# Kernel tuning notes

Measured on AMD Instinct MI355X. Metric: run time of the kernel, lower is better.

## Reference

```python
import jax, jax.numpy as jnp
import numpy as np

B, T, D, H = 4, 2048, 1024, 16
HD = D // H

def setup_inputs() -> dict:
    key = jax.random.key(0)
    ks = jax.random.split(key, 12)
    s = 0.02
    return {
        "query": jax.random.normal(ks[0], (B, T, D), dtype=jnp.float32),
        "key_": jax.random.normal(ks[1], (B, T, D), dtype=jnp.float32),
        "value": jax.random.normal(ks[2], (B, T, D), dtype=jnp.float32),
        "attention_mask": jnp.zeros((B, T, T), dtype=bool),
        "Wq": jax.random.normal(ks[3], (D, D), dtype=jnp.float32) * s,
        "bq": jnp.zeros((D,), dtype=jnp.float32),
        "Wk": jax.random.normal(ks[4], (D, D), dtype=jnp.float32) * s,
        "bk": jnp.zeros((D,), dtype=jnp.float32),
        "Wv": jax.random.normal(ks[5], (D, D), dtype=jnp.float32) * s,
        "bv": jnp.zeros((D,), dtype=jnp.float32),
        "Wo": jax.random.normal(ks[6], (D, D), dtype=jnp.float32) * s,
        "bo": jnp.zeros((D,), dtype=jnp.float32),
    }

def reference(query, key_, value, attention_mask, Wq, bq, Wk, bk, Wv, bv, Wo, bo):
    scale = 1.0 / jnp.sqrt(jnp.float32(HD))
    # projections (torch Linear: x @ W.T + b), split heads -> [B, H, T, HD]
    q = (query @ Wq.T + bq).reshape(B, T, H, HD).transpose(0, 2, 1, 3)
    k = (key_ @ Wk.T + bk).reshape(B, T, H, HD).transpose(0, 2, 1, 3)
    v = (value @ Wv.T + bv).reshape(B, T, H, HD).transpose(0, 2, 1, 3)
    scores = jnp.einsum('bhqd,bhkd->bhqk', q, k) * scale  # [B,H,T,T]
    mask = attention_mask[:, None, :, :]  # [B,1,T,T], True = masked
    scores = jnp.where(mask, -jnp.inf, scores)
    attn = jax.nn.softmax(scores, axis=-1)
    out = jnp.einsum('bhqk,bhkd->bhqd', attn, v)  # [B,H,T,HD]
    out = out.transpose(0, 2, 1, 3).reshape(B, T, D)
    return out @ Wo.T + bo
```

## Files before the change

### kernel.cpp

```cpp
#include <hip/hip_runtime.h>
#include <hip/hip_bf16.h>
#include <math.h>


typedef short bf16x8 __attribute__((ext_vector_type(8)));
typedef short bf16x4 __attribute__((ext_vector_type(4)));
typedef float f32x4  __attribute__((ext_vector_type(4)));
typedef float f32x16 __attribute__((ext_vector_type(16)));
typedef unsigned u32x4v __attribute__((ext_vector_type(4)));

#define DEV __device__ __forceinline__

DEV short f2bf(float f) {
    union { float f; unsigned u; } x; x.f = f;
    unsigned r = x.u + 0x7fffu + ((x.u >> 16) & 1u);
    return (short)(r >> 16);
}

DEV unsigned cvtpk(float lo, float hi) {
    unsigned r;
    asm("v_cvt_pk_bf16_f32 %0, %1, %2" : "=v"(r) : "v"(lo), "v"(hi));
    return r;
}

DEV void pl32swap(unsigned &a, unsigned &b) {
    asm volatile("v_permlane32_swap_b32 %0, %1" : "+v"(a), "+v"(b));
}

DEV float fexp2(float x) {
    float r;
    asm("v_exp_f32 %0, %1\n\ts_nop 0" : "=v"(r) : "v"(x));
    return r;
}

DEV void gload16(const void* g, void* lds_wave_base) {
    __builtin_amdgcn_global_load_lds(
        (const __attribute__((address_space(1))) void*)g,
        (__attribute__((address_space(3))) void*)lds_wave_base, 16, 0, 0);
}

DEV f32x4 mfma16(bf16x8 a, bf16x8 b, f32x4 c) {
    return __builtin_amdgcn_mfma_f32_16x16x32_bf16(a, b, c, 0, 0, 0);
}
DEV f32x16 mfma32(bf16x8 a, bf16x8 b, f32x16 c) {
    return __builtin_amdgcn_mfma_f32_32x32x16_bf16(a, b, c, 0, 0, 0);
}

__global__ __launch_bounds__(256) void cvt_one(const float* __restrict__ in,
                                               short* __restrict__ out) {
    int i = (blockIdx.x * 256 + threadIdx.x) * 8;
    f32x4 a = *(const f32x4*)(in + i);
    f32x4 b = *(const f32x4*)(in + i + 4);
    union { unsigned u[4]; bf16x8 v; } p;
    p.u[0] = cvtpk(a[0], a[1]); p.u[1] = cvtpk(a[2], a[3]);
    p.u[2] = cvtpk(b[0], b[1]); p.u[3] = cvtpk(b[2], b[3]);
    *(bf16x8*)(out + i) = p.v;
}

__global__ __launch_bounds__(256) void cvt_w4(
    const float* __restrict__ a, const float* __restrict__ b,
    const float* __restrict__ c, const float* __restrict__ d,
    short* __restrict__ oa, short* __restrict__ ob,
    short* __restrict__ oc, short* __restrict__ od) {
    const int sel = blockIdx.x >> 9;
    const float* in = sel == 0 ? a : sel == 1 ? b : sel == 2 ? c : d;
    short* out      = sel == 0 ? oa : sel == 1 ? ob : sel == 2 ? oc : od;
    int i = ((blockIdx.x & 511) * 256 + threadIdx.x) * 8;
    f32x4 x = *(const f32x4*)(in + i);
    f32x4 y = *(const f32x4*)(in + i + 4);
    union { unsigned u[4]; bf16x8 v; } p;
    p.u[0] = cvtpk(x[0], x[1]); p.u[1] = cvtpk(x[2], x[3]);
    p.u[2] = cvtpk(y[0], y[1]); p.u[3] = cvtpk(y[2], y[3]);
    *(bf16x8*)(out + i) = p.v;
}

template<int EPI>
__global__ __launch_bounds__(256) void gemm_bt(
    const short* __restrict__ A, const short* __restrict__ W,
    const float* __restrict__ bias, void* __restrict__ Cp, float epiScale)
{
    __shared__ short Alds[2][4096];
    __shared__ short Blds[2][4096];

    const int t = threadIdx.x;
    const int wave = t >> 6, lane = t & 63;
    const int lr = lane & 15, lg = lane >> 4;
    const int wg = (blockIdx.x & 7) * 64 + (blockIdx.x >> 3);
    const int m0 = (wg >> 3) * 128, n0 = (wg & 7) * 128;
    const int wr = wave >> 1, wc = wave & 1;

    const int o0 = t * 16,        kb0 = o0 >> 11, row0 = (o0 >> 4) & 127;
    const int o1 = 4096 + t * 16, kb1 = o1 >> 11, row1 = (o1 >> 4) & 127;
    const short* As0 = A + (size_t)(m0 + row0) * 1024 + kb0 * 8;
    const short* As1 = A + (size_t)(m0 + row1) * 1024 + kb1 * 8;
    const short* Ws0 = W + (size_t)(n0 + row0) * 1024 + kb0 * 8;
    const short* Ws1 = W + (size_t)(n0 + row1) * 1024 + kb1 * 8;

    auto stage = [&](short* dA, short* dB, int k0) {
        gload16(As0 + k0, (char*)dA + wave * 1024);
        gload16(As1 + k0, (char*)dA + 4096 + wave * 1024);
        gload16(Ws0 + k0, (char*)dB + wave * 1024);
        gload16(Ws1 + k0, (char*)dB + 4096 + wave * 1024);
    };

    f32x4 acc[4][4] = {};

    stage(Alds[0], Blds[0], 0);

    auto kstep = [&](int ts, int BUF) {
        if (ts < 31) {
            stage(Alds[BUF ^ 1], Blds[BUF ^ 1], (ts + 1) * 32);
            asm volatile("s_waitcnt vmcnt(4)" ::: "memory");
        } else {
            asm volatile("s_waitcnt vmcnt(0)" ::: "memory");
        }
        __builtin_amdgcn_s_barrier();
        bf16x8 af[4], bfr[4];
        #pragma unroll
        for (int mi = 0; mi < 4; mi++)
            af[mi] = *(const bf16x8*)(Alds[BUF] + lg * 1024 + (wr * 64 + mi * 16 + lr) * 8);
        #pragma unroll
        for (int ni = 0; ni < 4; ni++)
            bfr[ni] = *(const bf16x8*)(Blds[BUF] + lg * 1024 + (wc * 64 + ni * 16 + lr) * 8);
        #pragma unroll
        for (int mi = 0; mi < 4; mi++)
            #pragma unroll
            for (int ni = 0; ni < 4; ni++)
                acc[mi][ni] = mfma16(af[mi], bfr[ni], acc[mi][ni]);
        __builtin_amdgcn_s_barrier();
    };

    #pragma unroll 1
    for (int it = 0; it < 16; ++it) { kstep(2 * it, 0); kstep(2 * it + 1, 1); }

    #pragma unroll
    for (int mi = 0; mi < 4; mi++) {
        #pragma unroll
        for (int ni = 0; ni < 4; ni++) {
            const int n      = n0 + wc * 64 + ni * 16 + lr;
            const int m_base = m0 + wr * 64 + mi * 16 + lg * 4;
            const float bv   = bias[n];
            f32x4 a = acc[mi][ni];
            if constexpr (EPI == 0) {
                short* C = (short*)Cp;
                #pragma unroll
                for (int r = 0; r < 4; r++)
                    C[(size_t)(m_base + r) * 1024 + n] = f2bf((a[r] + bv) * epiScale);
            } else if constexpr (EPI == 2) {
                short* C = (short*)Cp;
                const int b = m_base >> 11, tt = m_base & 2047;
                bf16x4 p;
                #pragma unroll
                for (int r = 0; r < 4; r++) p[r] = f2bf(a[r] + bv);
                *(bf16x4*)(C + (size_t)b * 2097152 + (size_t)n * 2048 + tt) = p;
            } else {
                float* C = (float*)Cp;
                #pragma unroll
                for (int r = 0; r < 4; r++)
                    C[(size_t)(m_base + r) * 1024 + n] = a[r] + bv;
            }
        }
    }
}

__global__ __launch_bounds__(256) void mask_scan(const unsigned char* __restrict__ mask,
                                                 unsigned char* __restrict__ flags) {
    __shared__ int anyk[32];
    const int t = threadIdx.x, kt = t & 31, g = t >> 5;
    const int b = blockIdx.x >> 6, qt = blockIdx.x & 63;
    if (t < 32) anyk[t] = 0;
    __syncthreads();
    unsigned acc = 0;
    const unsigned char* base = mask + ((size_t)b * 2048 + qt * 32 + g * 4) * 2048 + kt * 64;
    #pragma unroll
    for (int rr = 0; rr < 4; rr++) {
        const uint4* p = (const uint4*)(base + (size_t)rr * 2048);
        #pragma unroll
        for (int s = 0; s < 4; s++) { uint4 v = p[s]; acc |= v.x | v.y | v.z | v.w; }
    }
    if (acc) anyk[kt] = 1;
    __syncthreads();
    if (t < 32) flags[((size_t)b * 64 + qt) * 32 + t] = (unsigned char)anyk[t];
}

__global__ __launch_bounds__(256, 2) void attn_fwd3(
    const short* __restrict__ Q, const short* __restrict__ K,
    const short* __restrict__ Vt, const unsigned char* __restrict__ mask,
    const unsigned char* __restrict__ flags, short* __restrict__ O)
{
    __shared__ short lds[2][2][8192];

    const int t = threadIdx.x, wave = t >> 6, lane = t & 63;
    const int j31 = lane & 31, hi = lane >> 5;

    const int raw = blockIdx.x;
    const int wg  = (raw & 7) * 128 + (raw >> 3);
    const int qblk = wg & 15, bh = wg >> 4;
    const int h = bh & 15, b = bh >> 4;
    const int q0 = qblk * 128 + wave * 32;

    bf16x8 qf[4];
    {
        const short* qp = Q + ((size_t)b * 2048 + q0 + j31) * 1024 + h * 64 + hi * 8;
        #pragma unroll
        for (int ck = 0; ck < 4; ck++) qf[ck] = *(const bf16x8*)(qp + ck * 16);
    }
    unsigned long long fmask;
    {
        unsigned char fb = flags[((size_t)b * 64 + qblk * 4 + wave) * 32 + j31];
        fmask = __ballot(fb != 0);
    }
    bf16x8 onesv;
    #pragma unroll
    for (int i = 0; i < 8; i++) onesv[i] = (short)0x3F80;

    const short* Kg = K + ((size_t)b * 2048) * 1024 + h * 64;
    const short* Vg = Vt + (size_t)b * 2097152 + (size_t)h * 64 * 2048;

    auto stage = [&](short* dK, short* dV, int tk) {
        #pragma unroll
        for (int i = 0; i < 4; i++) {
            const int s = i * 256 + t;
            const int rK = s >> 3, cK = ((s & 7) ^ (rK & 7)) * 8;
            gload16(Kg + (size_t)(tk + rK) * 1024 + cK, dK + i * 2048 + wave * 512);
            const int rV = s >> 4, cV = ((s & 15) ^ (rV & 15)) * 8;
            gload16(Vg + (size_t)rV * 2048 + tk + cV, dV + i * 2048 + wave * 512);
        }
    };

    stage(&lds[0][0][0], &lds[0][1][0], 0);

    f32x16 oA = {}, oB = {}, accL = {};
    float m = -1e30f;
    const int swk = j31 & 7, swv = j31 & 15;

    auto tile = [&](int J, int BUF) {
        if (J < 15) {
            stage(&lds[BUF ^ 1][0][0], &lds[BUF ^ 1][1][0], (J + 1) * 128);
            asm volatile("s_waitcnt vmcnt(8)" ::: "memory");
        } else {
            asm volatile("s_waitcnt vmcnt(0)" ::: "memory");
        }
        __builtin_amdgcn_s_barrier();
        const short* ldsK = &lds[BUF][0][0];
        const short* ldsV = &lds[BUF][1][0];

        f32x16 sA = {}, sB = {}, sC = {}, sD = {};
        __builtin_amdgcn_s_setprio(1);
        #pragma unroll
        for (int ck = 0; ck < 4; ck++) {
            const int co = ((2 * ck + hi) ^ swk) * 8;
            bf16x8 k0 = *(const bf16x8*)(ldsK + (j31      ) * 64 + co);
            bf16x8 k1 = *(const bf16x8*)(ldsK + (32 + j31) * 64 + co);
            bf16x8 k2 = *(const bf16x8*)(ldsK + (64 + j31) * 64 + co);
            bf16x8 k3 = *(const bf16x8*)(ldsK + (96 + j31) * 64 + co);
            sA = mfma32(k0, qf[ck], sA);
            sB = mfma32(k1, qf[ck], sB);
            sC = mfma32(k2, qf[ck], sC);
            sD = mfma32(k3, qf[ck], sD);
        }
        __builtin_amdgcn_s_setprio(0);

        if ((fmask >> (2 * J)) & 3ULL) {
            const unsigned char* mp = mask + ((size_t)b * 2048 + q0 + j31) * 2048
                                           + (size_t)J * 128 + hi * 4;
            auto apply = [&](f32x16& sX, int X) {
                #pragma unroll
                for (int rg = 0; rg < 4; rg++) {
                    unsigned mb = *(const unsigned*)(mp + X * 32 + rg * 8);
                    #pragma unroll
                    for (int e = 0; e < 4; e++)
                        if ((mb >> (8 * e)) & 0xFFu) sX[rg * 4 + e] = -1e30f;
                }
            };
            apply(sA, 0); apply(sB, 1); apply(sC, 2); apply(sD, 3);
        }

        float tm = fmaxf(sA[0], sA[1]);
        #pragma unroll
        for (int r = 2; r < 16; r += 2) tm = fmaxf(fmaxf(tm, sA[r]), sA[r + 1]);
        #pragma unroll
        for (int r = 0; r < 16; r += 2) tm = fmaxf(fmaxf(tm, sB[r]), sB[r + 1]);
        #pragma unroll
        for (int r = 0; r < 16; r += 2) tm = fmaxf(fmaxf(tm, sC[r]), sC[r + 1]);
        #pragma unroll
        for (int r = 0; r < 16; r += 2) tm = fmaxf(fmaxf(tm, sD[r]), sD[r + 1]);
        tm = fmaxf(tm, __shfl_xor(tm, 32));
        if (!__all(tm <= m + 8.f)) {
            const float mnew = fmaxf(m, tm);
            const float fs = fexp2(m - mnew);
            m = mnew;
            #pragma unroll
            for (int r = 0; r < 16; r++) { oA[r] *= fs; oB[r] *= fs; }
            accL[0] *= fs;
        }
        #pragma unroll
        for (int r = 0; r < 16; r++) sA[r] = fexp2(sA[r] - m);
        #pragma unroll
        for (int r = 0; r < 16; r++) sB[r] = fexp2(sB[r] - m);
        #pragma unroll
        for (int r = 0; r < 16; r++) sC[r] = fexp2(sC[r] - m);
        #pragma unroll
        for (int r = 0; r < 16; r++) sD[r] = fexp2(sD[r] - m);

        __builtin_amdgcn_s_setprio(1);
        #pragma unroll
        for (int c = 0; c < 8; c++) {
            const f32x16& sX = (c < 2) ? sA : (c < 4) ? sB : (c < 6) ? sC : sD;
            const int rb = 8 * (c & 1);
            unsigned A0 = cvtpk(sX[rb],     sX[rb + 1]), B0 = cvtpk(sX[rb + 4], sX[rb + 5]);
            unsigned A1 = cvtpk(sX[rb + 2], sX[rb + 3]), B1 = cvtpk(sX[rb + 6], sX[rb + 7]);
            pl32swap(A0, B0); pl32swap(A1, B1);
            union { unsigned u[4]; bf16x8 v; } pu;
            pu.u[0] = A0; pu.u[1] = A1; pu.u[2] = B0; pu.u[3] = B1;
            const int co = ((2 * c + hi) ^ swv) * 8;
            bf16x8 v0 = *(const bf16x8*)(ldsV + (j31      ) * 128 + co);
            bf16x8 v1 = *(const bf16x8*)(ldsV + (32 + j31) * 128 + co);
            oA   = mfma32(v0, pu.v, oA);
            oB   = mfma32(v1, pu.v, oB);
            accL = mfma32(onesv, pu.v, accL);
        }
        __builtin_amdgcn_s_setprio(0);
        __builtin_amdgcn_s_barrier();
    };

    #pragma unroll 1
    for (int jj = 0; jj < 8; ++jj) { tile(2 * jj, 0); tile(2 * jj + 1, 1); }

    __syncthreads();
    unsigned* ow = (unsigned*)&lds[0][0][0] + wave * (32 * 34);
    const float inv = 1.f / accL[0];
    #pragma unroll
    for (int o = 0; o < 2; o++)
        #pragma unroll
        for (int rp = 0; rp < 8; rp++) {
            const int r  = 2 * rp;
            const int hd = 2 * (rp & 1) + 8 * (rp >> 1) + 4 * hi + 32 * o;
            const float v0 = (o ? oB[r]     : oA[r])     * inv;
            const float v1 = (o ? oB[r + 1] : oA[r + 1]) * inv;
            ow[j31 * 34 + (hd >> 1)] = cvtpk(v0, v1);
        }
    __syncthreads();
    {
        const size_t orow = ((size_t)b * 2048 + q0 + j31) * 1024 + h * 64 + hi * 32;
        unsigned* gout = (unsigned*)(O + orow);
        const unsigned* src = ow + j31 * 34 + hi * 16;
        #pragma unroll
        for (int i = 0; i < 4; i++) {
            u32x4v v;
            v[0] = src[i*4]; v[1] = src[i*4+1]; v[2] = src[i*4+2]; v[3] = src[i*4+3];
            *(u32x4v*)(gout + i * 4) = v;
        }
    }
}

extern "C" void kernel_launch(void* const* d_in, const int* in_sizes, int n_in,
                              void* d_out, int out_size, void* d_ws, size_t ws_size,
                              hipStream_t stream)
{
    const float* query = (const float*)d_in[0];
    const float* key_  = (const float*)d_in[1];
    const float* value = (const float*)d_in[2];
    const unsigned char* amask = (const unsigned char*)d_in[3];
    const float* Wq = (const float*)d_in[4];
    const float* bq = (const float*)d_in[5];
    const float* Wk = (const float*)d_in[6];
    const float* bk = (const float*)d_in[7];
    const float* Wv = (const float*)d_in[8];
    const float* bv = (const float*)d_in[9];
    const float* Wo = (const float*)d_in[10];
    const float* bo = (const float*)d_in[11];
    float* out = (float*)d_out;

    char* ws = (char*)d_ws;
    const size_t MB = 1024 * 1024;
    short* Wqb = (short*)(ws + 0 * MB);
    short* Wkb = (short*)(ws + 2 * MB);
    short* Wvb = (short*)(ws + 4 * MB);
    short* Wob = (short*)(ws + 6 * MB);
    short* Qb  = (short*)(ws + 8 * MB);
    short* Kb  = (short*)(ws + 24 * MB);
    short* Vtb = (short*)(ws + 40 * MB);
    short* Xb  = (short*)(ws + 56 * MB);
    unsigned char* flagsb = (unsigned char*)(ws + 0 * MB);

    cvt_w4<<<2048, 256, 0, stream>>>(Wq, Wk, Wv, Wo, Wqb, Wkb, Wvb, Wob);

    const float qscale = 0.125f * 1.44269504088896f;
    cvt_one<<<4096, 256, 0, stream>>>(query, Xb);
    gemm_bt<0><<<512, 256, 0, stream>>>(Xb, Wqb, bq, Qb, qscale);
    cvt_one<<<4096, 256, 0, stream>>>(key_, Xb);
    gemm_bt<0><<<512, 256, 0, stream>>>(Xb, Wkb, bk, Kb, 1.0f);
    cvt_one<<<4096, 256, 0, stream>>>(value, Xb);
    gemm_bt<2><<<512, 256, 0, stream>>>(Xb, Wvb, bv, Vtb, 1.0f);

    mask_scan<<<256, 256, 0, stream>>>(amask, flagsb);

    attn_fwd3<<<1024, 256, 0, stream>>>(Qb, Kb, Vtb, amask, flagsb, Xb);

    gemm_bt<3><<<512, 256, 0, stream>>>(Xb, Wob, bo, out, 1.0f);
}
```

Baseline: 280.2 us.

## Use 256x256 GEMM tiles and split attention tile into two softmax halves

The projection GEMMs move from 128x128 tiles with 256 threads to 256x256 tiles with 512 threads and 8x4 accumulators per wave, so each block gets more operand reuse per LDS load. This launches only 128 blocks, which may underfill the 256 CUs. The attention kernel now computes the first two score blocks, masks them and starts their exponentials before issuing the QK MFMAs for the other two, so exp work can overlap matrix work. If the running max changes, the first half is recomputed. Barriers are wrapped in scheduling fences so the compiler cannot move work across them.

```diff
diff --git a/kernel.cpp b/kernel.cpp
--- a/kernel.cpp
+++ b/kernel.cpp
@@ -37,6 +37,12 @@
     __builtin_amdgcn_global_load_lds(
         (const __attribute__((address_space(1))) void*)g,
         (__attribute__((address_space(3))) void*)lds_wave_base, 16, 0, 0);
+}
+
+DEV void barrier_pinned() {
+    __builtin_amdgcn_sched_barrier(0);
+    __builtin_amdgcn_s_barrier();
+    __builtin_amdgcn_sched_barrier(0);
 }
 
 DEV f32x4 mfma16(bf16x8 a, bf16x8 b, f32x4 c) {
@@ -75,36 +81,35 @@
 }
 
 template<int EPI>
-__global__ __launch_bounds__(256) void gemm_bt(
+__global__ __launch_bounds__(512, 2) void gemm256(
     const short* __restrict__ A, const short* __restrict__ W,
     const float* __restrict__ bias, void* __restrict__ Cp, float epiScale)
 {
-    __shared__ short Alds[2][4096];
-    __shared__ short Blds[2][4096];
-
-    const int t = threadIdx.x;
-    const int wave = t >> 6, lane = t & 63;
+    __shared__ short Alds[2][8192];
+    __shared__ short Blds[2][8192];
+
+    const int t = threadIdx.x, wave = t >> 6, lane = t & 63;
     const int lr = lane & 15, lg = lane >> 4;
-    const int wg = (blockIdx.x & 7) * 64 + (blockIdx.x >> 3);
-    const int m0 = (wg >> 3) * 128, n0 = (wg & 7) * 128;
-    const int wr = wave >> 1, wc = wave & 1;
-
-    const int o0 = t * 16,        kb0 = o0 >> 11, row0 = (o0 >> 4) & 127;
-    const int o1 = 4096 + t * 16, kb1 = o1 >> 11, row1 = (o1 >> 4) & 127;
-    const short* As0 = A + (size_t)(m0 + row0) * 1024 + kb0 * 8;
-    const short* As1 = A + (size_t)(m0 + row1) * 1024 + kb1 * 8;
-    const short* Ws0 = W + (size_t)(n0 + row0) * 1024 + kb0 * 8;
-    const short* Ws1 = W + (size_t)(n0 + row1) * 1024 + kb1 * 8;
+    const int wg = (blockIdx.x & 7) * 16 + (blockIdx.x >> 3);
+    const int m0 = (wg >> 2) * 256, n0 = (wg & 3) * 256;
+    const int wr = wave >> 2, wc = wave & 3;
+
+    const int p0 = t, p1 = 512 + t;
+    const int kbA0 = p0 >> 8, rA0 = p0 & 255;
+    const int kbA1 = p1 >> 8, rA1 = p1 & 255;
+    const short* As0 = A + (size_t)(m0 + rA0) * 1024 + kbA0 * 8;
+    const short* As1 = A + (size_t)(m0 + rA1) * 1024 + kbA1 * 8;
+    const short* Ws0 = W + (size_t)(n0 + rA0) * 1024 + kbA0 * 8;
+    const short* Ws1 = W + (size_t)(n0 + rA1) * 1024 + kbA1 * 8;
 
     auto stage = [&](short* dA, short* dB, int k0) {
-        gload16(As0 + k0, (char*)dA + wave * 1024);
-        gload16(As1 + k0, (char*)dA + 4096 + wave * 1024);
-        gload16(Ws0 + k0, (char*)dB + wave * 1024);
-        gload16(Ws1 + k0, (char*)dB + 4096 + wave * 1024);
+        gload16(As0 + k0, (char*)dA +        wave * 1024);
+        gload16(As1 + k0, (char*)dA + 8192 + wave * 1024);
+        gload16(Ws0 + k0, (char*)dB +        wave * 1024);
+        gload16(Ws1 + k0, (char*)dB + 8192 + wave * 1024);
     };
 
-    f32x4 acc[4][4] = {};
-
+    f32x4 acc[8][4] = {};
     stage(Alds[0], Blds[0], 0);
 
     auto kstep = [&](int ts, int BUF) {
@@ -114,31 +119,31 @@
         } else {
             asm volatile("s_waitcnt vmcnt(0)" ::: "memory");
         }
-        __builtin_amdgcn_s_barrier();
-        bf16x8 af[4], bfr[4];
-        #pragma unroll
-        for (int mi = 0; mi < 4; mi++)
-            af[mi] = *(const bf16x8*)(Alds[BUF] + lg * 1024 + (wr * 64 + mi * 16 + lr) * 8);
+        barrier_pinned();
+        bf16x8 af[8], bfr[4];
+        #pragma unroll
+        for (int mi = 0; mi < 8; mi++)
+            af[mi] = *(const bf16x8*)(Alds[BUF] + (lg * 256 + wr * 128 + mi * 16 + lr) * 8);
         #pragma unroll
         for (int ni = 0; ni < 4; ni++)
-            bfr[ni] = *(const bf16x8*)(Blds[BUF] + lg * 1024 + (wc * 64 + ni * 16 + lr) * 8);
-        #pragma unroll
-        for (int mi = 0; mi < 4; mi++)
+            bfr[ni] = *(const bf16x8*)(Blds[BUF] + (lg * 256 + wc * 64 + ni * 16 + lr) * 8);
+        #pragma unroll
+        for (int mi = 0; mi < 8; mi++)
             #pragma unroll
             for (int ni = 0; ni < 4; ni++)
                 acc[mi][ni] = mfma16(af[mi], bfr[ni], acc[mi][ni]);
-        __builtin_amdgcn_s_barrier();
+        barrier_pinned();
     };
 
     #pragma unroll 1
     for (int it = 0; it < 16; ++it) { kstep(2 * it, 0); kstep(2 * it + 1, 1); }
 
     #pragma unroll
-    for (int mi = 0; mi < 4; mi++) {
+    for (int mi = 0; mi < 8; mi++) {
         #pragma unroll
         for (int ni = 0; ni < 4; ni++) {
             const int n      = n0 + wc * 64 + ni * 16 + lr;
-            const int m_base = m0 + wr * 64 + mi * 16 + lg * 4;
+            const int m_base = m0 + wr * 128 + mi * 16 + lg * 4;
             const float bv   = bias[n];
             f32x4 a = acc[mi][ni];
             if constexpr (EPI == 0) {
@@ -183,7 +188,7 @@
     if (t < 32) flags[((size_t)b * 64 + qt) * 32 + t] = (unsigned char)anyk[t];
 }
 
-__global__ __launch_bounds__(256, 2) void attn_fwd3(
+__global__ __launch_bounds__(256, 2) void attn_fwd5(
     const short* __restrict__ Q, const short* __restrict__ K,
     const short* __restrict__ Vt, const unsigned char* __restrict__ mask,
     const unsigned char* __restrict__ flags, short* __restrict__ O)
@@ -241,46 +246,69 @@
         } else {
             asm volatile("s_waitcnt vmcnt(0)" ::: "memory");
         }
-        __builtin_amdgcn_s_barrier();
+        barrier_pinned();
         const short* ldsK = &lds[BUF][0][0];
         const short* ldsV = &lds[BUF][1][0];
-
-        f32x16 sA = {}, sB = {}, sC = {}, sD = {};
+        const bool masked = ((fmask >> (2 * J)) & 3ULL) != 0;
+
+        f32x16 sA = {}, sB = {};
         __builtin_amdgcn_s_setprio(1);
         #pragma unroll
         for (int ck = 0; ck < 4; ck++) {
             const int co = ((2 * ck + hi) ^ swk) * 8;
             bf16x8 k0 = *(const bf16x8*)(ldsK + (j31      ) * 64 + co);
             bf16x8 k1 = *(const bf16x8*)(ldsK + (32 + j31) * 64 + co);
+            sA = mfma32(k0, qf[ck], sA);
+            sB = mfma32(k1, qf[ck], sB);
+        }
+        __builtin_amdgcn_s_setprio(0);
+        if (masked) {
+            const unsigned char* mp = mask + ((size_t)b * 2048 + q0 + j31) * 2048
+                                           + (size_t)J * 128 + hi * 4;
+            #pragma unroll
+            for (int rg = 0; rg < 4; rg++) {
+                unsigned ma = *(const unsigned*)(mp + rg * 8);
+                unsigned mb = *(const unsigned*)(mp + 32 + rg * 8);
+                #pragma unroll
+                for (int e = 0; e < 4; e++) {
+                    if ((ma >> (8 * e)) & 0xFFu) sA[rg * 4 + e] = -1e30f;
+                    if ((mb >> (8 * e)) & 0xFFu) sB[rg * 4 + e] = -1e30f;
+                }
+            }
+        }
+        float tmab = fmaxf(sA[0], sA[1]);
+        #pragma unroll
+        for (int r = 2; r < 16; r += 2) tmab = fmaxf(fmaxf(tmab, sA[r]), sA[r + 1]);
+        #pragma unroll
+        for (int r = 0; r < 16; r += 2) tmab = fmaxf(fmaxf(tmab, sB[r]), sB[r + 1]);
+        f32x16 pA, pB;
+        #pragma unroll
+        for (int r = 0; r < 16; r++) { pA[r] = fexp2(sA[r] - m); pB[r] = fexp2(sB[r] - m); }
+
+        f32x16 sC = {}, sD = {};
+        #pragma unroll
+        for (int ck = 0; ck < 4; ck++) {
+            const int co = ((2 * ck + hi) ^ swk) * 8;
             bf16x8 k2 = *(const bf16x8*)(ldsK + (64 + j31) * 64 + co);
             bf16x8 k3 = *(const bf16x8*)(ldsK + (96 + j31) * 64 + co);
-            sA = mfma32(k0, qf[ck], sA);
-            sB = mfma32(k1, qf[ck], sB);
             sC = mfma32(k2, qf[ck], sC);
             sD = mfma32(k3, qf[ck], sD);
         }
-        __builtin_amdgcn_s_setprio(0);
-
-        if ((fmask >> (2 * J)) & 3ULL) {
+        if (masked) {
             const unsigned char* mp = mask + ((size_t)b * 2048 + q0 + j31) * 2048
                                            + (size_t)J * 128 + hi * 4;
-            auto apply = [&](f32x16& sX, int X) {
+            #pragma unroll
+            for (int rg = 0; rg < 4; rg++) {
+                unsigned mc = *(const unsigned*)(mp + 64 + rg * 8);
+                unsigned md = *(const unsigned*)(mp + 96 + rg * 8);
                 #pragma unroll
-                for (int rg = 0; rg < 4; rg++) {
-                    unsigned mb = *(const unsigned*)(mp + X * 32 + rg * 8);
-                    #pragma unroll
-                    for (int e = 0; e < 4; e++)
-                        if ((mb >> (8 * e)) & 0xFFu) sX[rg * 4 + e] = -1e30f;
+                for (int e = 0; e < 4; e++) {
+                    if ((mc >> (8 * e)) & 0xFFu) sC[rg * 4 + e] = -1e30f;
+                    if ((md >> (8 * e)) & 0xFFu) sD[rg * 4 + e] = -1e30f;
                 }
-            };
-            apply(sA, 0); apply(sB, 1); apply(sC, 2); apply(sD, 3);
-        }
-
-        float tm = fmaxf(sA[0], sA[1]);
-        #pragma unroll
-        for (int r = 2; r < 16; r += 2) tm = fmaxf(fmaxf(tm, sA[r]), sA[r + 1]);
-        #pragma unroll
-        for (int r = 0; r < 16; r += 2) tm = fmaxf(fmaxf(tm, sB[r]), sB[r + 1]);
+            }
+        }
+        float tm = tmab;
         #pragma unroll
         for (int r = 0; r < 16; r += 2) tm = fmaxf(fmaxf(tm, sC[r]), sC[r + 1]);
         #pragma unroll
@@ -291,22 +319,18 @@
             const float fs = fexp2(m - mnew);
             m = mnew;
             #pragma unroll
+            for (int r = 0; r < 16; r++) { pA[r] = fexp2(sA[r] - m); pB[r] = fexp2(sB[r] - m); }
+            #pragma unroll
             for (int r = 0; r < 16; r++) { oA[r] *= fs; oB[r] *= fs; }
             accL[0] *= fs;
         }
         #pragma unroll
-        for (int r = 0; r < 16; r++) sA[r] = fexp2(sA[r] - m);
-        #pragma unroll
-        for (int r = 0; r < 16; r++) sB[r] = fexp2(sB[r] - m);
-        #pragma unroll
-        for (int r = 0; r < 16; r++) sC[r] = fexp2(sC[r] - m);
-        #pragma unroll
-        for (int r = 0; r < 16; r++) sD[r] = fexp2(sD[r] - m);
+        for (int r = 0; r < 16; r++) { sC[r] = fexp2(sC[r] - m); sD[r] = fexp2(sD[r] - m); }
 
         __builtin_amdgcn_s_setprio(1);
         #pragma unroll
         for (int c = 0; c < 8; c++) {
-            const f32x16& sX = (c < 2) ? sA : (c < 4) ? sB : (c < 6) ? sC : sD;
+            const f32x16& sX = (c < 2) ? pA : (c < 4) ? pB : (c < 6) ? sC : sD;
             const int rb = 8 * (c & 1);
             unsigned A0 = cvtpk(sX[rb],     sX[rb + 1]), B0 = cvtpk(sX[rb + 4], sX[rb + 5]);
             unsigned A1 = cvtpk(sX[rb + 2], sX[rb + 3]), B1 = cvtpk(sX[rb + 6], sX[rb + 7]);
@@ -321,7 +345,7 @@
             accL = mfma32(onesv, pu.v, accL);
         }
         __builtin_amdgcn_s_setprio(0);
-        __builtin_amdgcn_s_barrier();
+        barrier_pinned();
     };
 
     #pragma unroll 1
@@ -388,15 +412,15 @@
 
     const float qscale = 0.125f * 1.44269504088896f;
     cvt_one<<<4096, 256, 0, stream>>>(query, Xb);
-    gemm_bt<0><<<512, 256, 0, stream>>>(Xb, Wqb, bq, Qb, qscale);
+    gemm256<0><<<128, 512, 0, stream>>>(Xb, Wqb, bq, Qb, qscale);
     cvt_one<<<4096, 256, 0, stream>>>(key_, Xb);
-    gemm_bt<0><<<512, 256, 0, stream>>>(Xb, Wkb, bk, Kb, 1.0f);
+    gemm256<0><<<128, 512, 0, stream>>>(Xb, Wkb, bk, Kb, 1.0f);
     cvt_one<<<4096, 256, 0, stream>>>(value, Xb);
-    gemm_bt<2><<<512, 256, 0, stream>>>(Xb, Wvb, bv, Vtb, 1.0f);
+    gemm256<2><<<128, 512, 0, stream>>>(Xb, Wvb, bv, Vtb, 1.0f);
 
     mask_scan<<<256, 256, 0, stream>>>(amask, flagsb);
 
-    attn_fwd3<<<1024, 256, 0, stream>>>(Qb, Kb, Vtb, amask, flagsb, Xb);
-
-    gemm_bt<3><<<512, 256, 0, stream>>>(Xb, Wob, bo, out, 1.0f);
-}
+    attn_fwd5<<<1024, 256, 0, stream>>>(Qb, Kb, Vtb, amask, flagsb, Xb);
+
+    gemm256<3><<<128, 512, 0, stream>>>(Xb, Wob, bo, out, 1.0f);
+}
```

After: 329.5 us. 1.18x slower.
